# Optimization experiments

Measured on AMD Instinct MI355X. Metric: run time of the kernel, lower is better.

Reference implementation:

```python
import jax, jax.numpy as jnp
import numpy as np

N, E, D, H = 50000, 800000, 128, 8
HD = D // H  # head dim = 16


def setup_inputs() -> dict:
    key = jax.random.key(0)
    ks = jax.random.split(key, 9)
    x = jax.random.normal(ks[0], (N, D), dtype=jnp.float32)
    edge_index = jax.random.randint(ks[1], (2, E), 0, N, dtype=jnp.int64)
    s = 0.05
    Wq = jax.random.normal(ks[2], (D, D), dtype=jnp.float32) * s
    bq = jax.random.normal(ks[3], (D,), dtype=jnp.float32) * s
    Wk = jax.random.normal(ks[4], (D, D), dtype=jnp.float32) * s
    bk = jax.random.normal(ks[5], (D,), dtype=jnp.float32) * s
    Wv = jax.random.normal(ks[6], (D, D), dtype=jnp.float32) * s
    bv = jax.random.normal(ks[7], (D,), dtype=jnp.float32) * s
    return {"x": x, "Wq": Wq, "bq": bq, "Wk": Wk, "bk": bk, "Wv": Wv, "bv": bv,
            "edge_index": edge_index}


def reference(x, Wq, bq, Wk, bk, Wv, bv, edge_index):
    n = x.shape[0]
    # Linear projections (torch Linear: x @ W.T + b), split into heads
    Q = (x @ Wq.T + bq).reshape(n, H, HD)  # [N,H,hd]
    K = (x @ Wk.T + bk).reshape(n, H, HD)
    V = (x @ Wv.T + bv).reshape(n, H, HD)
    src, dst = edge_index[0], edge_index[1]
    # per-edge attention score: sum over head dim of K[src]*Q[dst]/sqrt(hd), clamp, exp
    score = jnp.sum(K[src] * Q[dst], axis=-1, keepdims=True) / np.sqrt(HD)  # [E,H,1]
    score = jnp.exp(jnp.clip(score, -5.0, 5.0))
    msg = V[src] * score  # [E,H,hd]
    wV = jax.ops.segment_sum(msg, dst, num_segments=n)      # [N,H,hd]
    Z = jax.ops.segment_sum(score, dst, num_segments=n)     # [N,H,1]
    h_out = wV / (Z + 1e-6)
    return h_out.reshape(n, H * HD)
```

## Files before the change

### kernel.cpp

```cpp
#include <hip/hip_runtime.h>
#include <hip/hip_bf16.h>

#define NN 50000
#define EE 800000
#define DD 128
#define HH 8
#define CAP 64
#define KVS 256
#define QB 391
#define PAB 196
#define NBIN 196
#define RSTRIDE 4096

typedef short bf16x8 __attribute__((ext_vector_type(8)));
typedef float f32x4 __attribute__((ext_vector_type(4)));
typedef unsigned short ushort8_t __attribute__((ext_vector_type(8)));

__device__ __forceinline__ unsigned short f2b(float f) {
    unsigned int u = __builtin_bit_cast(unsigned int, f);
    unsigned int r = (u + 0x7FFFu + ((u >> 16) & 1u)) >> 16;
    return (unsigned short)r;
}
__device__ __forceinline__ float b2f(unsigned short u) {
    return __builtin_bit_cast(float, ((unsigned int)u) << 16);
}

__global__ __launch_bounds__(256) void prep(const float* __restrict__ Wq,
                                            const float* __restrict__ Wk,
                                            const float* __restrict__ Wv,
                                            unsigned short* __restrict__ Wqb,
                                            unsigned short* __restrict__ Wkb,
                                            unsigned short* __restrict__ Wvb) {
    int idx = blockIdx.x * 256 + threadIdx.x;
    int mat = idx >> 12;
    int off = idx & 4095;
    const float* src = (mat == 0) ? Wq : (mat == 1) ? Wk : Wv;
    unsigned short* dst = (mat == 0) ? Wqb : (mat == 1) ? Wkb : Wvb;
    float4 v = ((const float4*)src)[off];
    ushort4 o;
    o.x = f2b(v.x); o.y = f2b(v.y); o.z = f2b(v.z); o.w = f2b(v.w);
    ((ushort4*)dst)[off] = o;
}

template <int OUTKIND>
__device__ __forceinline__ void qkv_mat(const unsigned short* __restrict__ W,
                                        const float* __restrict__ bias,
                                        float* __restrict__ qo,
                                        unsigned short* __restrict__ kvo,
                                        int kvoff,
                                        const bf16x8 a[2][4],
                                        int r0, int mrow, int kb,
                                        bool act0, bool act1) {
#pragma unroll
    for (int c0 = 0; c0 < 8; ++c0) {
        float bval = bias[c0 * 16 + mrow];
        const unsigned short* wr = W + (size_t)(c0 * 16 + mrow) * DD + kb * 8;
        bf16x8 w0 = *(const bf16x8*)(wr);
        bf16x8 w1 = *(const bf16x8*)(wr + 32);
        bf16x8 w2 = *(const bf16x8*)(wr + 64);
        bf16x8 w3 = *(const bf16x8*)(wr + 96);
#pragma unroll
        for (int g = 0; g < 2; ++g) {
            bool act = (g == 0) ? act0 : act1;
            f32x4 acc = {bval, bval, bval, bval};
            acc = __builtin_amdgcn_mfma_f32_16x16x32_bf16(a[g][0], w0, acc, 0, 0, 0);
            acc = __builtin_amdgcn_mfma_f32_16x16x32_bf16(a[g][1], w1, acc, 0, 0, 0);
            acc = __builtin_amdgcn_mfma_f32_16x16x32_bf16(a[g][2], w2, acc, 0, 0, 0);
            acc = __builtin_amdgcn_mfma_f32_16x16x32_bf16(a[g][3], w3, acc, 0, 0, 0);
            if (act) {
                int orow = r0 + 16 * g + kb * 4;
                int col = c0 * 16 + mrow;
                if (OUTKIND == 0) {
#pragma unroll
                    for (int r = 0; r < 4; ++r)
                        qo[(size_t)(orow + r) * DD + col] = acc[r];
                } else {
#pragma unroll
                    for (int r = 0; r < 4; ++r)
                        kvo[(size_t)(orow + r) * KVS + kvoff + col] = f2b(acc[r]);
                }
            }
        }
    }
}

__global__ __launch_bounds__(256) void mega(
    const float* __restrict__ x,
    const unsigned short* __restrict__ Wq, const float* __restrict__ bq,
    const unsigned short* __restrict__ Wk, const float* __restrict__ bk,
    const unsigned short* __restrict__ Wv, const float* __restrict__ bv,
    const int* __restrict__ ei,
    float* __restrict__ Qo, unsigned short* __restrict__ KV,
    int* __restrict__ runbuf, int* __restrict__ gcount,
    int* __restrict__ gstart) {
    __shared__ int lcnt[256];
    __shared__ int lpre[256];
    if (blockIdx.x < QB) {
        const int wave = threadIdx.x >> 6;
        const int l = threadIdx.x & 63;
        const int r0 = blockIdx.x * 128 + wave * 32;
        const int mrow = l & 15;
        const int kb = l >> 4;
        const bool act0 = (r0 < NN);
        const bool act1 = (r0 + 16 < NN);
        if (!act0) return;

        bf16x8 a[2][4];
#pragma unroll
        for (int g = 0; g < 2; ++g) {
            int row = (g == 0 || act1) ? (r0 + 16 * g + mrow) : r0;
            const float* xr = x + (size_t)row * DD + kb * 8;
#pragma unroll
            for (int s = 0; s < 4; ++s) {
                float4 f0 = *(const float4*)(xr + s * 32);
                float4 f1 = *(const float4*)(xr + s * 32 + 4);
                bf16x8 t;
                t[0] = (short)f2b(f0.x); t[1] = (short)f2b(f0.y);
                t[2] = (short)f2b(f0.z); t[3] = (short)f2b(f0.w);
                t[4] = (short)f2b(f1.x); t[5] = (short)f2b(f1.y);
                t[6] = (short)f2b(f1.z); t[7] = (short)f2b(f1.w);
                a[g][s] = t;
            }
        }
        qkv_mat<0>(Wq, bq, Qo, (unsigned short*)nullptr, 0, a, r0, mrow, kb, act0, act1);
        qkv_mat<1>(Wk, bk, (float*)nullptr, KV, 0,   a, r0, mrow, kb, act0, act1);
        qkv_mat<1>(Wv, bv, (float*)nullptr, KV, 128, a, r0, mrow, kb, act0, act1);
    } else {
        const int b = blockIdx.x - QB;
        const int t = threadIdx.x;
        lcnt[t] = 0;
        __syncthreads();

        int ss[16], dd[16], slot[16];
        int base4 = b * 1024 + t;
#pragma unroll
        for (int j = 0; j < 4; ++j) {
            int idx = base4 + j * 256;
            int4 sv = make_int4(0, 0, 0, 0);
            int4 dv = make_int4(-1, -1, -1, -1);
            if (idx < EE / 4) {
                sv = ((const int4*)ei)[idx];
                dv = ((const int4*)(ei + EE))[idx];
            }
            ss[j * 4 + 0] = sv.x; ss[j * 4 + 1] = sv.y;
            ss[j * 4 + 2] = sv.z; ss[j * 4 + 3] = sv.w;
            dd[j * 4 + 0] = dv.x; dd[j * 4 + 1] = dv.y;
            dd[j * 4 + 2] = dv.z; dd[j * 4 + 3] = dv.w;
        }
#pragma unroll
        for (int k = 0; k < 16; ++k)
            slot[k] = (dd[k] >= 0) ? atomicAdd(&lcnt[dd[k] >> 8], 1) : 0;
        __syncthreads();

        int myCnt = lcnt[t];
        lpre[t] = myCnt;
        __syncthreads();
        for (int off = 1; off < 256; off <<= 1) {
            int v = (t >= off) ? lpre[t - off] : 0;
            __syncthreads();
            lpre[t] += v;
            __syncthreads();
        }
        int excl = lpre[t] - myCnt;
        __syncthreads();
        lpre[t] = excl;
        __syncthreads();

#pragma unroll
        for (int k = 0; k < 16; ++k) {
            if (dd[k] >= 0) {
                int pos = b * RSTRIDE + lpre[dd[k] >> 8] + slot[k];
                runbuf[pos] = ss[k] | ((dd[k] & 255) << 16);
            }
        }
        if (t < NBIN) {
            gcount[t * PAB + b] = myCnt;
            gstart[t * PAB + b] = excl;
        }
    }
}

__global__ __launch_bounds__(256) void binscatter(const int* __restrict__ runbuf,
                                                  const int* __restrict__ gcount,
                                                  const int* __restrict__ gstart,
                                                  int* __restrict__ cnt,
                                                  unsigned short* __restrict__ bucket) {
    __shared__ int cnt2[256];
    const int c = blockIdx.x, t = threadIdx.x;
    cnt2[t] = 0;
    __syncthreads();
    if (t < PAB) {
        int start = gstart[c * PAB + t];
        int count = gcount[c * PAB + t];
        const int* run = runbuf + t * RSTRIDE + start;
        for (int i = 0; i < count; ++i) {
            int e = run[i];
            int dloc = (e >> 16) & 255;
            int p = atomicAdd(&cnt2[dloc], 1);
            if (p < CAP)
                bucket[(size_t)(c * 256 + dloc) * CAP + p] = (unsigned short)(e & 0xFFFF);
        }
    }
    __syncthreads();
    int node = c * 256 + t;
    if (node < NN) cnt[node] = cnt2[t];
}

__global__ __launch_bounds__(128) void gather8(const unsigned short* __restrict__ KV,
                                               const int* __restrict__ cnt,
                                               const unsigned short* __restrict__ bucket,
                                               float* __restrict__ qout) {
    int n = blockIdx.x * 2 + (threadIdx.x >> 6);
    if (n >= NN) return;
    int l = threadIdx.x & 63;
    int es = l >> 3;
    int h = l & 7;

    int mySrc = (int)bucket[(size_t)n * CAP + l];
    int d = cnt[n];
    const float4* qp = (const float4*)(qout + (size_t)n * DD + 16 * h);
    float4 q0 = qp[0], q1 = qp[1], q2 = qp[2], q3 = qp[3];
    float qf[16] = {q0.x, q0.y, q0.z, q0.w, q1.x, q1.y, q1.z, q1.w,
                    q2.x, q2.y, q2.z, q2.w, q3.x, q3.y, q3.z, q3.w};

    float acc[16];
#pragma unroll
    for (int j = 0; j < 16; ++j) acc[j] = 0.f;
    float z = 0.f;
    d = min(d, CAP);

    for (int i = 0; i < d; i += 8) {
        int eidx = i + es;
        bool valid = eidx < d;
        int src = __shfl(mySrc, valid ? eidx : i);
        const unsigned short* kr = KV + (size_t)src * KVS + 16 * h;
        ushort8_t k0 = *(const ushort8_t*)kr;
        ushort8_t k1 = *(const ushort8_t*)(kr + 8);
        ushort8_t v0 = *(const ushort8_t*)(kr + 128);
        ushort8_t v1 = *(const ushort8_t*)(kr + 136);
        float s = qf[0] * b2f(k0[0]) + qf[1] * b2f(k0[1]) +
                  qf[2] * b2f(k0[2]) + qf[3] * b2f(k0[3]) +
                  qf[4] * b2f(k0[4]) + qf[5] * b2f(k0[5]) +
                  qf[6] * b2f(k0[6]) + qf[7] * b2f(k0[7]) +
                  qf[8] * b2f(k1[0]) + qf[9] * b2f(k1[1]) +
                  qf[10] * b2f(k1[2]) + qf[11] * b2f(k1[3]) +
                  qf[12] * b2f(k1[4]) + qf[13] * b2f(k1[5]) +
                  qf[14] * b2f(k1[6]) + qf[15] * b2f(k1[7]);
        s *= 0.25f;
        s = fminf(fmaxf(s, -5.f), 5.f);
        s = __expf(s);
        if (!valid) s = 0.f;
#pragma unroll
        for (int j = 0; j < 8; ++j) acc[j] += b2f(v0[j]) * s;
#pragma unroll
        for (int j = 0; j < 8; ++j) acc[8 + j] += b2f(v1[j]) * s;
        z += s;
    }
#pragma unroll
    for (int m = 8; m <= 32; m <<= 1) {
#pragma unroll
        for (int j = 0; j < 16; ++j) acc[j] += __shfl_xor(acc[j], m);
        z += __shfl_xor(z, m);
    }
    if (es == 0) {
        float inv = 1.f / (z + 1e-6f);
        float4* orow = (float4*)(qout + (size_t)n * DD + 16 * h);
#pragma unroll
        for (int j = 0; j < 4; ++j)
            orow[j] = make_float4(acc[4 * j] * inv, acc[4 * j + 1] * inv,
                                  acc[4 * j + 2] * inv, acc[4 * j + 3] * inv);
    }
}

extern "C" void kernel_launch(void* const* d_in, const int* in_sizes, int n_in,
                              void* d_out, int out_size, void* d_ws, size_t ws_size,
                              hipStream_t stream) {
    const float* x  = (const float*)d_in[0];
    const float* Wq = (const float*)d_in[1];
    const float* bq = (const float*)d_in[2];
    const float* Wk = (const float*)d_in[3];
    const float* bk = (const float*)d_in[4];
    const float* Wv = (const float*)d_in[5];
    const float* bv = (const float*)d_in[6];
    const int*   ei = (const int*)d_in[7];
    float* out = (float*)d_out;

    unsigned short* KV  = (unsigned short*)d_ws;
    unsigned short* Wqb = KV + (size_t)NN * KVS;
    unsigned short* Wkb = Wqb + DD * DD;
    unsigned short* Wvb = Wkb + DD * DD;
    int* cnt = (int*)(Wvb + DD * DD);
    unsigned short* bucket = (unsigned short*)(cnt + NN);
    int* runbuf = (int*)(bucket + (size_t)NN * CAP);
    int* gcount = runbuf + (size_t)PAB * RSTRIDE;
    int* gstart = gcount + NBIN * PAB;

    prep<<<48, 256, 0, stream>>>(Wq, Wk, Wv, Wqb, Wkb, Wvb);
    mega<<<QB + PAB, 256, 0, stream>>>(x, Wqb, bq, Wkb, bk, Wvb, bv, ei,
                                       out, KV, runbuf, gcount, gstart);
    binscatter<<<NBIN, 256, 0, stream>>>(runbuf, gcount, gstart, cnt, bucket);
    gather8<<<(NN + 1) / 2, 128, 0, stream>>>(KV, cnt, bucket, out);
}
```

Before: 118.2 us.

## Regroup launches to overlap bin-scatter with QKV projection and store Q as bf16

Weight conversion and the edge partitioning pass now share one launch, and the bin-scatter runs in the same launch as the QKV MFMA projection, so the stages overlap and the pipeline drops from four kernel launches to three. Q is now written as bf16 into its own workspace buffer instead of fp32 into the output, which halves Q write and read traffic. The gather kernel then writes to the output directly. In exchange Q loses precision before the score dot product, and the workspace grows by an N x D bf16 buffer.

New measurement: 107.2 us. 1.1x faster.

```diff
diff --git a/kernel.cpp b/kernel.cpp
--- a/kernel.cpp
+++ b/kernel.cpp
@@ -7,7 +7,7 @@
 #define HH 8
 #define CAP 64
 #define KVS 256
-#define QB 391
+#define QKB 391
 #define PAB 196
 #define NBIN 196
 #define RSTRIDE 4096
@@ -25,29 +25,87 @@
     return __builtin_bit_cast(float, ((unsigned int)u) << 16);
 }
 
-__global__ __launch_bounds__(256) void prep(const float* __restrict__ Wq,
-                                            const float* __restrict__ Wk,
-                                            const float* __restrict__ Wv,
-                                            unsigned short* __restrict__ Wqb,
-                                            unsigned short* __restrict__ Wkb,
-                                            unsigned short* __restrict__ Wvb) {
-    int idx = blockIdx.x * 256 + threadIdx.x;
-    int mat = idx >> 12;
-    int off = idx & 4095;
-    const float* src = (mat == 0) ? Wq : (mat == 1) ? Wk : Wv;
-    unsigned short* dst = (mat == 0) ? Wqb : (mat == 1) ? Wkb : Wvb;
-    float4 v = ((const float4*)src)[off];
-    ushort4 o;
-    o.x = f2b(v.x); o.y = f2b(v.y); o.z = f2b(v.z); o.w = f2b(v.w);
-    ((ushort4*)dst)[off] = o;
-}
-
-template <int OUTKIND>
+__global__ __launch_bounds__(256) void prepA(const float* __restrict__ Wq,
+                                             const float* __restrict__ Wk,
+                                             const float* __restrict__ Wv,
+                                             unsigned short* __restrict__ Wqb,
+                                             unsigned short* __restrict__ Wkb,
+                                             unsigned short* __restrict__ Wvb,
+                                             const int* __restrict__ ei,
+                                             int* __restrict__ runbuf,
+                                             int* __restrict__ gcount,
+                                             int* __restrict__ gstart) {
+    __shared__ int lcnt[256];
+    __shared__ int lpre[256];
+    if (blockIdx.x < 48) {
+        int idx = blockIdx.x * 256 + threadIdx.x;
+        int mat = idx >> 12;
+        int off = idx & 4095;
+        const float* src = (mat == 0) ? Wq : (mat == 1) ? Wk : Wv;
+        unsigned short* dst = (mat == 0) ? Wqb : (mat == 1) ? Wkb : Wvb;
+        float4 v = ((const float4*)src)[off];
+        ushort4 o;
+        o.x = f2b(v.x); o.y = f2b(v.y); o.z = f2b(v.z); o.w = f2b(v.w);
+        ((ushort4*)dst)[off] = o;
+    } else {
+        const int b = blockIdx.x - 48;
+        const int t = threadIdx.x;
+        lcnt[t] = 0;
+        __syncthreads();
+
+        int ss[16], dd[16], slot[16];
+        int base4 = b * 1024 + t;
+#pragma unroll
+        for (int j = 0; j < 4; ++j) {
+            int idx = base4 + j * 256;
+            int4 sv = make_int4(0, 0, 0, 0);
+            int4 dv = make_int4(-1, -1, -1, -1);
+            if (idx < EE / 4) {
+                sv = ((const int4*)ei)[idx];
+                dv = ((const int4*)(ei + EE))[idx];
+            }
+            ss[j * 4 + 0] = sv.x; ss[j * 4 + 1] = sv.y;
+            ss[j * 4 + 2] = sv.z; ss[j * 4 + 3] = sv.w;
+            dd[j * 4 + 0] = dv.x; dd[j * 4 + 1] = dv.y;
+            dd[j * 4 + 2] = dv.z; dd[j * 4 + 3] = dv.w;
+        }
+#pragma unroll
+        for (int k = 0; k < 16; ++k)
+            slot[k] = (dd[k] >= 0) ? atomicAdd(&lcnt[dd[k] >> 8], 1) : 0;
+        __syncthreads();
+
+        int myCnt = lcnt[t];
+        lpre[t] = myCnt;
+        __syncthreads();
+        for (int off = 1; off < 256; off <<= 1) {
+            int v = (t >= off) ? lpre[t - off] : 0;
+            __syncthreads();
+            lpre[t] += v;
+            __syncthreads();
+        }
+        int excl = lpre[t] - myCnt;
+        __syncthreads();
+        lpre[t] = excl;
+        __syncthreads();
+
+#pragma unroll
+        for (int k = 0; k < 16; ++k) {
+            if (dd[k] >= 0) {
+                int pos = b * RSTRIDE + lpre[dd[k] >> 8] + slot[k];
+                runbuf[pos] = ss[k] | ((dd[k] & 255) << 16);
+            }
+        }
+        if (t < NBIN) {
+            gcount[t * PAB + b] = myCnt;
+            gstart[t * PAB + b] = excl;
+        }
+    }
+}
+
 __device__ __forceinline__ void qkv_mat(const unsigned short* __restrict__ W,
                                         const float* __restrict__ bias,
-                                        float* __restrict__ qo,
-                                        unsigned short* __restrict__ kvo,
-                                        int kvoff,
+                                        unsigned short* __restrict__ outp,
+                                        int stride, int off,
                                         const bf16x8 a[2][4],
                                         int r0, int mrow, int kb,
                                         bool act0, bool act1) {
@@ -70,35 +128,49 @@
             if (act) {
                 int orow = r0 + 16 * g + kb * 4;
                 int col = c0 * 16 + mrow;
-                if (OUTKIND == 0) {
-#pragma unroll
-                    for (int r = 0; r < 4; ++r)
-                        qo[(size_t)(orow + r) * DD + col] = acc[r];
-                } else {
-#pragma unroll
-                    for (int r = 0; r < 4; ++r)
-                        kvo[(size_t)(orow + r) * KVS + kvoff + col] = f2b(acc[r]);
-                }
-            }
-        }
-    }
-}
-
-__global__ __launch_bounds__(256) void mega(
+#pragma unroll
+                for (int r = 0; r < 4; ++r)
+                    outp[(size_t)(orow + r) * stride + off + col] = f2b(acc[r]);
+            }
+        }
+    }
+}
+
+__global__ __launch_bounds__(256) void qkvbin(
     const float* __restrict__ x,
     const unsigned short* __restrict__ Wq, const float* __restrict__ bq,
     const unsigned short* __restrict__ Wk, const float* __restrict__ bk,
     const unsigned short* __restrict__ Wv, const float* __restrict__ bv,
-    const int* __restrict__ ei,
-    float* __restrict__ Qo, unsigned short* __restrict__ KV,
-    int* __restrict__ runbuf, int* __restrict__ gcount,
-    int* __restrict__ gstart) {
-    __shared__ int lcnt[256];
-    __shared__ int lpre[256];
-    if (blockIdx.x < QB) {
+    unsigned short* __restrict__ Qb, unsigned short* __restrict__ KV,
+    const int* __restrict__ runbuf, const int* __restrict__ gcount,
+    const int* __restrict__ gstart, int* __restrict__ cnt,
+    unsigned short* __restrict__ bucket) {
+    __shared__ int cnt2[256];
+    if (blockIdx.x < NBIN) {
+        const int c = blockIdx.x, t = threadIdx.x;
+        cnt2[t] = 0;
+        __syncthreads();
+        if (t < PAB) {
+            int start = gstart[c * PAB + t];
+            int count = gcount[c * PAB + t];
+            const int* run = runbuf + t * RSTRIDE + start;
+            for (int i = 0; i < count; ++i) {
+                int e = run[i];
+                int dloc = (e >> 16) & 255;
+                int p = atomicAdd(&cnt2[dloc], 1);
+                if (p < CAP)
+                    bucket[(size_t)(c * 256 + dloc) * CAP + p] =
+                        (unsigned short)(e & 0xFFFF);
+            }
+        }
+        __syncthreads();
+        int node = c * 256 + t;
+        if (node < NN) cnt[node] = cnt2[t];
+    } else {
+        const int b = blockIdx.x - NBIN;
         const int wave = threadIdx.x >> 6;
         const int l = threadIdx.x & 63;
-        const int r0 = blockIdx.x * 128 + wave * 32;
+        const int r0 = b * 128 + wave * 32;
         const int mrow = l & 15;
         const int kb = l >> 4;
         const bool act0 = (r0 < NN);
@@ -122,94 +194,17 @@
                 a[g][s] = t;
             }
         }
-        qkv_mat<0>(Wq, bq, Qo, (unsigned short*)nullptr, 0, a, r0, mrow, kb, act0, act1);
-        qkv_mat<1>(Wk, bk, (float*)nullptr, KV, 0,   a, r0, mrow, kb, act0, act1);
-        qkv_mat<1>(Wv, bv, (float*)nullptr, KV, 128, a, r0, mrow, kb, act0, act1);
-    } else {
-        const int b = blockIdx.x - QB;
-        const int t = threadIdx.x;
-        lcnt[t] = 0;
-        __syncthreads();
-
-        int ss[16], dd[16], slot[16];
-        int base4 = b * 1024 + t;
-#pragma unroll
-        for (int j = 0; j < 4; ++j) {
-            int idx = base4 + j * 256;
-            int4 sv = make_int4(0, 0, 0, 0);
-            int4 dv = make_int4(-1, -1, -1, -1);
-            if (idx < EE / 4) {
-                sv = ((const int4*)ei)[idx];
-                dv = ((const int4*)(ei + EE))[idx];
-            }
-            ss[j * 4 + 0] = sv.x; ss[j * 4 + 1] = sv.y;
-            ss[j * 4 + 2] = sv.z; ss[j * 4 + 3] = sv.w;
-            dd[j * 4 + 0] = dv.x; dd[j * 4 + 1] = dv.y;
-            dd[j * 4 + 2] = dv.z; dd[j * 4 + 3] = dv.w;
-        }
-#pragma unroll
-        for (int k = 0; k < 16; ++k)
-            slot[k] = (dd[k] >= 0) ? atomicAdd(&lcnt[dd[k] >> 8], 1) : 0;
-        __syncthreads();
-
-        int myCnt = lcnt[t];
-        lpre[t] = myCnt;
-        __syncthreads();
-        for (int off = 1; off < 256; off <<= 1) {
-            int v = (t >= off) ? lpre[t - off] : 0;
-            __syncthreads();
-            lpre[t] += v;
-            __syncthreads();
-        }
-        int excl = lpre[t] - myCnt;
-        __syncthreads();
-        lpre[t] = excl;
-        __syncthreads();
-
-#pragma unroll
-        for (int k = 0; k < 16; ++k) {
-            if (dd[k] >= 0) {
-                int pos = b * RSTRIDE + lpre[dd[k] >> 8] + slot[k];
-                runbuf[pos] = ss[k] | ((dd[k] & 255) << 16);
-            }
-        }
-        if (t < NBIN) {
-            gcount[t * PAB + b] = myCnt;
-            gstart[t * PAB + b] = excl;
-        }
-    }
-}
-
-__global__ __launch_bounds__(256) void binscatter(const int* __restrict__ runbuf,
-                                                  const int* __restrict__ gcount,
-                                                  const int* __restrict__ gstart,
-                                                  int* __restrict__ cnt,
-                                                  unsigned short* __restrict__ bucket) {
-    __shared__ int cnt2[256];
-    const int c = blockIdx.x, t = threadIdx.x;
-    cnt2[t] = 0;
-    __syncthreads();
-    if (t < PAB) {
-        int start = gstart[c * PAB + t];
-        int count = gcount[c * PAB + t];
-        const int* run = runbuf + t * RSTRIDE + start;
-        for (int i = 0; i < count; ++i) {
-            int e = run[i];
-            int dloc = (e >> 16) & 255;
-            int p = atomicAdd(&cnt2[dloc], 1);
-            if (p < CAP)
-                bucket[(size_t)(c * 256 + dloc) * CAP + p] = (unsigned short)(e & 0xFFFF);
-        }
-    }
-    __syncthreads();
-    int node = c * 256 + t;
-    if (node < NN) cnt[node] = cnt2[t];
+        qkv_mat(Wq, bq, Qb, DD, 0,    a, r0, mrow, kb, act0, act1);
+        qkv_mat(Wk, bk, KV, KVS, 0,   a, r0, mrow, kb, act0, act1);
+        qkv_mat(Wv, bv, KV, KVS, 128, a, r0, mrow, kb, act0, act1);
+    }
 }
 
 __global__ __launch_bounds__(128) void gather8(const unsigned short* __restrict__ KV,
+                                               const unsigned short* __restrict__ Qb,
                                                const int* __restrict__ cnt,
                                                const unsigned short* __restrict__ bucket,
-                                               float* __restrict__ qout) {
+                                               float* __restrict__ outp) {
     int n = blockIdx.x * 2 + (threadIdx.x >> 6);
     if (n >= NN) return;
     int l = threadIdx.x & 63;
@@ -218,10 +213,14 @@
 
     int mySrc = (int)bucket[(size_t)n * CAP + l];
     int d = cnt[n];
-    const float4* qp = (const float4*)(qout + (size_t)n * DD + 16 * h);
-    float4 q0 = qp[0], q1 = qp[1], q2 = qp[2], q3 = qp[3];
-    float qf[16] = {q0.x, q0.y, q0.z, q0.w, q1.x, q1.y, q1.z, q1.w,
-                    q2.x, q2.y, q2.z, q2.w, q3.x, q3.y, q3.z, q3.w};
+    const unsigned short* qp = Qb + (size_t)n * DD + 16 * h;
+    ushort8_t qu0 = *(const ushort8_t*)qp;
+    ushort8_t qu1 = *(const ushort8_t*)(qp + 8);
+    float qf[16];
+#pragma unroll
+    for (int j = 0; j < 8; ++j) qf[j] = b2f(qu0[j]);
+#pragma unroll
+    for (int j = 0; j < 8; ++j) qf[8 + j] = b2f(qu1[j]);
 
     float acc[16];
 #pragma unroll
@@ -264,7 +263,7 @@
     }
     if (es == 0) {
         float inv = 1.f / (z + 1e-6f);
-        float4* orow = (float4*)(qout + (size_t)n * DD + 16 * h);
+        float4* orow = (float4*)(outp + (size_t)n * DD + 16 * h);
 #pragma unroll
         for (int j = 0; j < 4; ++j)
             orow[j] = make_float4(acc[4 * j] * inv, acc[4 * j + 1] * inv,
@@ -286,7 +285,8 @@
     float* out = (float*)d_out;
 
     unsigned short* KV  = (unsigned short*)d_ws;
-    unsigned short* Wqb = KV + (size_t)NN * KVS;
+    unsigned short* Qb  = KV + (size_t)NN * KVS;
+    unsigned short* Wqb = Qb + (size_t)NN * DD;
     unsigned short* Wkb = Wqb + DD * DD;
     unsigned short* Wvb = Wkb + DD * DD;
     int* cnt = (int*)(Wvb + DD * DD);
@@ -295,9 +295,10 @@
     int* gcount = runbuf + (size_t)PAB * RSTRIDE;
     int* gstart = gcount + NBIN * PAB;
 
-    prep<<<48, 256, 0, stream>>>(Wq, Wk, Wv, Wqb, Wkb, Wvb);
-    mega<<<QB + PAB, 256, 0, stream>>>(x, Wqb, bq, Wkb, bk, Wvb, bv, ei,
-                                       out, KV, runbuf, gcount, gstart);
-    binscatter<<<NBIN, 256, 0, stream>>>(runbuf, gcount, gstart, cnt, bucket);
-    gather8<<<(NN + 1) / 2, 128, 0, stream>>>(KV, cnt, bucket, out);
-}
+    prepA<<<48 + PAB, 256, 0, stream>>>(Wq, Wk, Wv, Wqb, Wkb, Wvb, ei,
+                                        runbuf, gcount, gstart);
+    qkvbin<<<NBIN + QKB, 256, 0, stream>>>(x, Wqb, bq, Wkb, bk, Wvb, bv,
+                                           Qb, KV, runbuf, gcount, gstart,
+                                           cnt, bucket);
+    gather8<<<(NN + 1) / 2, 128, 0, stream>>>(KV, Qb, cnt, bucket, out);
+}
```
